# Optimization experiments

Hardware: AMD Instinct MI355X
Metric: run time of the kernel (lower is better)

The kernel has to match this reference:

```python
import jax, jax.numpy as jnp
import numpy as np

BITS = 8
GROUP_SIZE = 32


def setup_inputs() -> dict:
    key = jax.random.key(0)
    k_x, k_w, k_b = jax.random.split(key, 3)
    out_f, in_f = 4096, 4096
    num_groups = in_f // GROUP_SIZE
    x = jax.random.normal(k_x, (4, 2048, in_f), dtype=jnp.float32)
    orig_weight = jax.random.normal(k_w, (out_f, in_f), dtype=jnp.float32)
    value = jnp.zeros((out_f, in_f), dtype=jnp.float32)
    min_scale = jnp.ones((out_f, num_groups), dtype=jnp.float32)
    max_scale = jnp.ones((out_f, num_groups), dtype=jnp.float32)
    bias = jax.random.normal(k_b, (out_f,), dtype=jnp.float32)
    return {"x": x, "orig_weight": orig_weight, "value": value,
            "min_scale": min_scale, "max_scale": max_scale, "bias": bias}


def _dequant_weight(orig_weight, value, min_scale, max_scale):
    out_f, in_f = orig_weight.shape
    num_groups = in_f // GROUP_SIZE
    max_val = (1 << BITS) - 1
    wg = orig_weight.reshape(out_f, num_groups, GROUP_SIZE)
    w_min = jnp.min(wg, axis=-1, keepdims=True) * min_scale[..., None]
    w_max = jnp.max(wg, axis=-1, keepdims=True) * max_scale[..., None]
    scale = jnp.maximum((w_max - w_min) / max_val, 1e-8)
    zero_point = -w_min / scale
    ws = wg / scale + zero_point + value.reshape(out_f, num_groups, GROUP_SIZE)
    wq = jnp.clip(jnp.round(ws), 0.0, float(max_val))
    return (scale * (wq - zero_point)).reshape(out_f, in_f)


def reference(x, orig_weight, value, min_scale, max_scale, bias):
    # group-wise learnable fake-quant dequantization of the weight, then linear
    weight_dq = _dequant_weight(orig_weight, value, min_scale, max_scale)  # [out, in]
    return jnp.einsum('bsi,oi->bso', x, weight_dq) + bias
```

## Files before the change

kernel.cpp:

```cpp
#include <hip/hip_runtime.h>

#define M_DIM 8192
#define N_DIM 4096
#define K_DIM 4096
#define GROUPS_PER_ROW 128
#define NT (K_DIM / 64)

typedef short bf16x8 __attribute__((ext_vector_type(8)));
typedef float f32x4  __attribute__((ext_vector_type(4)));
typedef unsigned short u16x8 __attribute__((ext_vector_type(8)));

__device__ __forceinline__ unsigned short f2bf(float f) {
    unsigned int u = __float_as_uint(f);
    u += 0x7fffu + ((u >> 16) & 1u);
    return (unsigned short)(u >> 16);
}

typedef const __attribute__((address_space(1))) void gvoid_t;
typedef __attribute__((address_space(3))) void lvoid_t;
__device__ __forceinline__ void gload_lds16(const void* g, void* l) {
    __builtin_amdgcn_global_load_lds((gvoid_t*)g, (lvoid_t*)l, 16, 0, 0);
}

__global__ __launch_bounds__(256) void dequant_kernel(
        const float* __restrict__ w, const float* __restrict__ value,
        const float* __restrict__ mins, const float* __restrict__ maxs,
        unsigned short* __restrict__ wq) {
    int g = blockIdx.x * 256 + threadIdx.x;
    const float4* wp = reinterpret_cast<const float4*>(w + (size_t)g * 32);
    const float4* vp = reinterpret_cast<const float4*>(value + (size_t)g * 32);
    float4 wv[8], vv[8];
    #pragma unroll
    for (int j = 0; j < 8; j++) { wv[j] = wp[j]; vv[j] = vp[j]; }
    float mn = wv[0].x, mx = wv[0].x;
    #pragma unroll
    for (int j = 0; j < 8; j++) {
        mn = fminf(mn, fminf(fminf(wv[j].x, wv[j].y), fminf(wv[j].z, wv[j].w)));
        mx = fmaxf(mx, fmaxf(fmaxf(wv[j].x, wv[j].y), fmaxf(wv[j].z, wv[j].w)));
    }
    float w_min = mn * mins[g];
    float w_max = mx * maxs[g];
    float scale = fmaxf((w_max - w_min) * (1.0f / 255.0f), 1e-8f);
    float zp    = -w_min / scale;
    float rs    = 1.0f / scale;
    unsigned short ob[32];
    #pragma unroll
    for (int j = 0; j < 8; j++) {
        const float* wf = &wv[j].x;
        const float* vf = &vv[j].x;
        #pragma unroll
        for (int c = 0; c < 4; c++) {
            float ws_ = wf[c] * rs + zp + vf[c];
            float q   = fminf(fmaxf(rintf(ws_), 0.0f), 255.0f);
            ob[j * 4 + c] = f2bf(scale * (q - zp));
        }
    }
    u16x8* op = reinterpret_cast<u16x8*>(wq + (size_t)g * 32);
    #pragma unroll
    for (int j = 0; j < 4; j++) {
        u16x8 v;
        #pragma unroll
        for (int c = 0; c < 8; c++) v[c] = ob[j * 8 + c];
        op[j] = v;
    }
}

__global__ __launch_bounds__(256) void xconv_kernel(
        const float* __restrict__ x, unsigned short* __restrict__ xb) {
    int t = blockIdx.x * 256 + threadIdx.x;
    const float4* xp = reinterpret_cast<const float4*>(x) + (size_t)t * 2;
    float4 a = xp[0], b = xp[1];
    u16x8 v;
    v[0] = f2bf(a.x); v[1] = f2bf(a.y); v[2] = f2bf(a.z); v[3] = f2bf(a.w);
    v[4] = f2bf(b.x); v[5] = f2bf(b.y); v[6] = f2bf(b.z); v[7] = f2bf(b.w);
    reinterpret_cast<u16x8*>(xb)[t] = v;
}

__global__ __launch_bounds__(512, 2) void gemm_kernel(
        const unsigned short* __restrict__ A, const unsigned short* __restrict__ B,
        const float* __restrict__ bias, float* __restrict__ C) {
    __shared__ __align__(128) char lds[131072];

    const int tid  = threadIdx.x;
    const int lane = tid & 63;
    const int w    = tid >> 6;
    const int wr   = w >> 2;
    const int wc   = w & 3;
    const int l15  = lane & 15, lk = lane >> 4;

    const int bid = blockIdx.x;
    const int swz = (bid & 7) * 64 + (bid >> 3);
    const int bm  = swz >> 4;
    const int bn  = swz & 15;

    const int swb   = ((l15 >> 3) & 1) << 5;
    const int rbyte = ((l15 * 64 + lk * 16) ^ swb);
    const int abase = wr * 16384 + rbyte;
    const int bbase = 32768 + (wc >> 1) * 16384 + (wc & 1) * 4096 + rbyte;

    const int c0  = tid * 16;
    const int c1  = 8192 + tid * 16;
    const int lb0 = c0 ^ (((c0 >> 9) & 1) << 5);
    const int lb1 = c1 ^ (((c1 >> 9) & 1) << 5);
    const int so0 = ((lb0 >> 6) & 127) * (K_DIM * 2) + (lb0 >> 13) * 64 + (lb0 & 63);
    const int so1 = ((lb1 >> 6) & 127) * (K_DIM * 2) + (lb1 >> 13) * 64 + (lb1 & 63);

    const char* srcA0 = (const char*)A + (size_t)(bm * 256 +   0) * (K_DIM * 2);
    const char* srcA1 = (const char*)A + (size_t)(bm * 256 + 128) * (K_DIM * 2);
    const char* srcB0 = (const char*)B + (size_t)(bn * 256 +   0) * (K_DIM * 2);
    const char* srcB1 = (const char*)B + (size_t)(bn * 256 + 128) * (K_DIM * 2);

    char* ldsc = (char*)lds;
    auto STAGE = [&](const char* src, int tt, int regionOff) {
        gload_lds16(src + (size_t)tt * 128 + so0, ldsc + regionOff + c0);
        gload_lds16(src + (size_t)tt * 128 + so1, ldsc + regionOff + c1);
    };

    f32x4 acc[8][4] = {};
    bf16x8 af[4][2], bf_[4][2];

    STAGE(srcA0, 0, 0);
    STAGE(srcA1, 0, 16384);
    STAGE(srcB0, 0, 32768);
    STAGE(srcB1, 0, 49152);
    STAGE(srcA0, 1, 65536);
    STAGE(srcA1, 1, 65536 + 16384);
    asm volatile("s_waitcnt vmcnt(4)" ::: "memory");
    __builtin_amdgcn_s_barrier();
    __builtin_amdgcn_sched_barrier(0);

    #pragma unroll 2
    for (int t = 0; t < NT; ++t) {
        const int bo  = (t & 1) << 16;
        const int bo2 = bo ^ 65536;

        #pragma unroll
        for (int mi = 0; mi < 4; ++mi)
            #pragma unroll
            for (int kk = 0; kk < 2; ++kk)
                af[mi][kk] = *(const bf16x8*)(ldsc + bo + abase + mi * 1024 + kk * 8192);
        #pragma unroll
        for (int ni = 0; ni < 2; ++ni)
            #pragma unroll
            for (int kk = 0; kk < 2; ++kk)
                bf_[ni][kk] = *(const bf16x8*)(ldsc + bo + bbase + ni * 1024 + kk * 8192);
        if (t + 1 < NT) STAGE(srcB0, t + 1, bo2 + 32768);
        __builtin_amdgcn_s_barrier();
        __builtin_amdgcn_sched_barrier(0);
        __builtin_amdgcn_s_setprio(1);
        #pragma unroll
        for (int mi = 0; mi < 4; ++mi)
            #pragma unroll
            for (int ni = 0; ni < 2; ++ni)
                #pragma unroll
                for (int kk = 0; kk < 2; ++kk)
                    acc[mi][ni] = __builtin_amdgcn_mfma_f32_16x16x32_bf16(
                        af[mi][kk], bf_[ni][kk], acc[mi][ni], 0, 0, 0);
        __builtin_amdgcn_s_setprio(0);

        #pragma unroll
        for (int ni = 2; ni < 4; ++ni)
            #pragma unroll
            for (int kk = 0; kk < 2; ++kk)
                bf_[ni][kk] = *(const bf16x8*)(ldsc + bo + bbase + ni * 1024 + kk * 8192);
        if (t + 1 < NT) STAGE(srcB1, t + 1, bo2 + 49152);
        __builtin_amdgcn_s_barrier();
        __builtin_amdgcn_sched_barrier(0);
        __builtin_amdgcn_s_setprio(1);
        #pragma unroll
        for (int mi = 0; mi < 4; ++mi)
            #pragma unroll
            for (int ni = 2; ni < 4; ++ni)
                #pragma unroll
                for (int kk = 0; kk < 2; ++kk)
                    acc[mi][ni] = __builtin_amdgcn_mfma_f32_16x16x32_bf16(
                        af[mi][kk], bf_[ni][kk], acc[mi][ni], 0, 0, 0);
        __builtin_amdgcn_s_setprio(0);

        #pragma unroll
        for (int mi = 0; mi < 4; ++mi)
            #pragma unroll
            for (int kk = 0; kk < 2; ++kk)
                af[mi][kk] = *(const bf16x8*)(ldsc + bo + abase + 4096 + mi * 1024 + kk * 8192);
        if (t + 2 < NT) {
            STAGE(srcA0, t + 2, bo + 0);
            STAGE(srcA1, t + 2, bo + 16384);
        }
        __builtin_amdgcn_s_barrier();
        __builtin_amdgcn_sched_barrier(0);
        __builtin_amdgcn_s_setprio(1);
        #pragma unroll
        for (int mi = 0; mi < 4; ++mi)
            #pragma unroll
            for (int ni = 2; ni < 4; ++ni)
                #pragma unroll
                for (int kk = 0; kk < 2; ++kk)
                    acc[mi + 4][ni] = __builtin_amdgcn_mfma_f32_16x16x32_bf16(
                        af[mi][kk], bf_[ni][kk], acc[mi + 4][ni], 0, 0, 0);
        #pragma unroll
        for (int mi = 0; mi < 4; ++mi)
            #pragma unroll
            for (int ni = 0; ni < 2; ++ni)
                #pragma unroll
                for (int kk = 0; kk < 2; ++kk)
                    acc[mi + 4][ni] = __builtin_amdgcn_mfma_f32_16x16x32_bf16(
                        af[mi][kk], bf_[ni][kk], acc[mi + 4][ni], 0, 0, 0);
        __builtin_amdgcn_s_setprio(0);
        if (t + 2 < NT)      { asm volatile("s_waitcnt vmcnt(4)" ::: "memory"); }
        else if (t + 1 < NT) { asm volatile("s_waitcnt vmcnt(0)" ::: "memory"); }
        __builtin_amdgcn_s_barrier();
        __builtin_amdgcn_sched_barrier(0);
    }

    float bv[4];
    #pragma unroll
    for (int ni = 0; ni < 4; ++ni)
        bv[ni] = bias[bn * 256 + wc * 64 + ni * 16 + l15];
    #pragma unroll
    for (int mi = 0; mi < 8; ++mi) {
        const int m0 = bm * 256 + wr * 128 + mi * 16 + lk * 4;
        #pragma unroll
        for (int ni = 0; ni < 4; ++ni) {
            const int n = bn * 256 + wc * 64 + ni * 16 + l15;
            #pragma unroll
            for (int r = 0; r < 4; ++r)
                C[(size_t)(m0 + r) * N_DIM + n] = acc[mi][ni][r] + bv[ni];
        }
    }
}

__global__ __launch_bounds__(256) void fallback_gemm(
        const float* __restrict__ x, const float* __restrict__ w,
        const float* __restrict__ value, const float* __restrict__ mins,
        const float* __restrict__ maxs, const float* __restrict__ bias,
        float* __restrict__ out) {
    const int n = blockIdx.x;
    __shared__ float wrow[K_DIM];
    const int tid = threadIdx.x;
    if (tid < GROUPS_PER_ROW) {
        const int g = tid;
        const float* wp = w + (size_t)n * K_DIM + g * 32;
        const float* vp = value + (size_t)n * K_DIM + g * 32;
        float tw[32];
        float mn = 1e30f, mx = -1e30f;
        #pragma unroll
        for (int j = 0; j < 32; j++) {
            tw[j] = wp[j]; mn = fminf(mn, tw[j]); mx = fmaxf(mx, tw[j]);
        }
        float wmin = mn * mins[n * GROUPS_PER_ROW + g];
        float wmax = mx * maxs[n * GROUPS_PER_ROW + g];
        float scale = fmaxf((wmax - wmin) * (1.0f / 255.0f), 1e-8f);
        float zp = -wmin / scale;
        #pragma unroll
        for (int j = 0; j < 32; j++) {
            float ws_ = tw[j] / scale + zp + vp[j];
            float q = fminf(fmaxf(rintf(ws_), 0.0f), 255.0f);
            wrow[g * 32 + j] = scale * (q - zp);
        }
    }
    __syncthreads();
    const float bv = bias[n];
    for (int m = tid; m < M_DIM; m += 256) {
        const float4* xr = reinterpret_cast<const float4*>(x + (size_t)m * K_DIM);
        const float4* wr4 = reinterpret_cast<const float4*>(wrow);
        float s = 0.f;
        for (int k = 0; k < K_DIM / 4; k++) {
            float4 a = xr[k], b = wr4[k];
            s += a.x * b.x + a.y * b.y + a.z * b.z + a.w * b.w;
        }
        out[(size_t)m * N_DIM + n] = s + bv;
    }
}

extern "C" void kernel_launch(void* const* d_in, const int* in_sizes, int n_in,
                              void* d_out, int out_size, void* d_ws, size_t ws_size,
                              hipStream_t stream) {
    const float* x     = (const float*)d_in[0];
    const float* ow    = (const float*)d_in[1];
    const float* value = (const float*)d_in[2];
    const float* mins  = (const float*)d_in[3];
    const float* maxs  = (const float*)d_in[4];
    const float* bias  = (const float*)d_in[5];
    float* out = (float*)d_out;

    const size_t xb_bytes = (size_t)M_DIM * K_DIM * 2;
    const size_t wb_bytes = (size_t)N_DIM * K_DIM * 2;

    if (ws_size >= xb_bytes + wb_bytes) {
        unsigned short* xb = (unsigned short*)d_ws;
        unsigned short* wb = (unsigned short*)((char*)d_ws + xb_bytes);

        dequant_kernel<<<(N_DIM * GROUPS_PER_ROW) / 256, 256, 0, stream>>>(
            ow, value, mins, maxs, wb);
        xconv_kernel<<<(M_DIM * K_DIM / 8) / 256, 256, 0, stream>>>(x, xb);
        gemm_kernel<<<(M_DIM / 256) * (N_DIM / 256), 512, 0, stream>>>(
            xb, wb, bias, out);
    } else {
        fallback_gemm<<<N_DIM, 256, 0, stream>>>(x, ow, value, mins, maxs, bias, out);
    }
}
```

Baseline: 288.5 us.

## Switch GEMM inner tiles from 16x16x32 to 32x32x16 bf16 MFMA

Replaces the 16x16x32 MFMA micro-tiles with 32x32x16 MFMA instructions, reorganizing per-wave accumulators into 4x2 blocks of 16-float vectors and rewriting the LDS fragment addressing and swizzle for the new operand layout. The larger MFMA shape needs fewer LDS fragment reads per FLOP and fewer instructions, aiming to reduce LDS bandwidth pressure and issue overhead. The epilogue store mapping is updated to the 32x32 output layout. It risks LDS bank conflicts under the new access pattern and different register pressure.

```diff
diff --git a/kernel.cpp b/kernel.cpp
--- a/kernel.cpp
+++ b/kernel.cpp
@@ -7,7 +7,7 @@
 #define NT (K_DIM / 64)
 
 typedef short bf16x8 __attribute__((ext_vector_type(8)));
-typedef float f32x4  __attribute__((ext_vector_type(4)));
+typedef float f32x16 __attribute__((ext_vector_type(16)));
 typedef unsigned short u16x8 __attribute__((ext_vector_type(8)));
 
 __device__ __forceinline__ unsigned short f2bf(float f) {
@@ -86,17 +86,18 @@
     const int w    = tid >> 6;
     const int wr   = w >> 2;
     const int wc   = w & 3;
-    const int l15  = lane & 15, lk = lane >> 4;
+    const int l31  = lane & 31, l5 = lane >> 5;
 
     const int bid = blockIdx.x;
     const int swz = (bid & 7) * 64 + (bid >> 3);
     const int bm  = swz >> 4;
     const int bn  = swz & 15;
 
-    const int swb   = ((l15 >> 3) & 1) << 5;
-    const int rbyte = ((l15 * 64 + lk * 16) ^ swb);
-    const int abase = wr * 16384 + rbyte;
-    const int bbase = 32768 + (wc >> 1) * 16384 + (wc & 1) * 4096 + rbyte;
+    const int amask = (l31 & 8) << 2;
+    const int ib    = l5 * 16;
+
+    const int aoff = wr * 16384 + l31 * 64;
+    const int boff = 32768 + (wc >> 1) * 16384 + (wc & 1) * 4096 + l31 * 64;
 
     const int c0  = tid * 16;
     const int c1  = 8192 + tid * 16;
@@ -116,8 +117,9 @@
         gload_lds16(src + (size_t)tt * 128 + so1, ldsc + regionOff + c1);
     };
 
-    f32x4 acc[8][4] = {};
-    bf16x8 af[4][2], bf_[4][2];
+    f32x16 acc[4][2] = {};
+    bf16x8 af[2][4], bfA[4], bfB[4];
+
 
     STAGE(srcA0, 0, 0);
     STAGE(srcA1, 0, 16384);
@@ -135,53 +137,49 @@
         const int bo2 = bo ^ 65536;
 
         #pragma unroll
-        for (int mi = 0; mi < 4; ++mi)
-            #pragma unroll
-            for (int kk = 0; kk < 2; ++kk)
-                af[mi][kk] = *(const bf16x8*)(ldsc + bo + abase + mi * 1024 + kk * 8192);
-        #pragma unroll
-        for (int ni = 0; ni < 2; ++ni)
-            #pragma unroll
-            for (int kk = 0; kk < 2; ++kk)
-                bf_[ni][kk] = *(const bf16x8*)(ldsc + bo + bbase + ni * 1024 + kk * 8192);
+        for (int mb = 0; mb < 2; ++mb)
+            #pragma unroll
+            for (int kb = 0; kb < 4; ++kb)
+                af[mb][kb] = *(const bf16x8*)(ldsc + bo + aoff + mb * 2048
+                                + (kb >> 1) * 8192 + (((kb & 1) * 32) ^ amask) + ib);
+        #pragma unroll
+        for (int kb = 0; kb < 4; ++kb)
+            bfA[kb] = *(const bf16x8*)(ldsc + bo + boff
+                                + (kb >> 1) * 8192 + (((kb & 1) * 32) ^ amask) + ib);
         if (t + 1 < NT) STAGE(srcB0, t + 1, bo2 + 32768);
         __builtin_amdgcn_s_barrier();
         __builtin_amdgcn_sched_barrier(0);
         __builtin_amdgcn_s_setprio(1);
         #pragma unroll
-        for (int mi = 0; mi < 4; ++mi)
-            #pragma unroll
-            for (int ni = 0; ni < 2; ++ni)
-                #pragma unroll
-                for (int kk = 0; kk < 2; ++kk)
-                    acc[mi][ni] = __builtin_amdgcn_mfma_f32_16x16x32_bf16(
-                        af[mi][kk], bf_[ni][kk], acc[mi][ni], 0, 0, 0);
+        for (int mb = 0; mb < 2; ++mb)
+            #pragma unroll
+            for (int kb = 0; kb < 4; ++kb)
+                acc[mb][0] = __builtin_amdgcn_mfma_f32_32x32x16_bf16(
+                    af[mb][kb], bfA[kb], acc[mb][0], 0, 0, 0);
         __builtin_amdgcn_s_setprio(0);
 
         #pragma unroll
-        for (int ni = 2; ni < 4; ++ni)
-            #pragma unroll
-            for (int kk = 0; kk < 2; ++kk)
-                bf_[ni][kk] = *(const bf16x8*)(ldsc + bo + bbase + ni * 1024 + kk * 8192);
+        for (int kb = 0; kb < 4; ++kb)
+            bfB[kb] = *(const bf16x8*)(ldsc + bo + boff + 2048
+                                + (kb >> 1) * 8192 + (((kb & 1) * 32) ^ amask) + ib);
         if (t + 1 < NT) STAGE(srcB1, t + 1, bo2 + 49152);
         __builtin_amdgcn_s_barrier();
         __builtin_amdgcn_sched_barrier(0);
         __builtin_amdgcn_s_setprio(1);
         #pragma unroll
-        for (int mi = 0; mi < 4; ++mi)
-            #pragma unroll
-            for (int ni = 2; ni < 4; ++ni)
-                #pragma unroll
-                for (int kk = 0; kk < 2; ++kk)
-                    acc[mi][ni] = __builtin_amdgcn_mfma_f32_16x16x32_bf16(
-                        af[mi][kk], bf_[ni][kk], acc[mi][ni], 0, 0, 0);
+        for (int mb = 0; mb < 2; ++mb)
+            #pragma unroll
+            for (int kb = 0; kb < 4; ++kb)
+                acc[mb][1] = __builtin_amdgcn_mfma_f32_32x32x16_bf16(
+                    af[mb][kb], bfB[kb], acc[mb][1], 0, 0, 0);
         __builtin_amdgcn_s_setprio(0);
 
         #pragma unroll
-        for (int mi = 0; mi < 4; ++mi)
-            #pragma unroll
-            for (int kk = 0; kk < 2; ++kk)
-                af[mi][kk] = *(const bf16x8*)(ldsc + bo + abase + 4096 + mi * 1024 + kk * 8192);
+        for (int mb = 0; mb < 2; ++mb)
+            #pragma unroll
+            for (int kb = 0; kb < 4; ++kb)
+                af[mb][kb] = *(const bf16x8*)(ldsc + bo + aoff + (mb + 2) * 2048
+                                + (kb >> 1) * 8192 + (((kb & 1) * 32) ^ amask) + ib);
         if (t + 2 < NT) {
             STAGE(srcA0, t + 2, bo + 0);
             STAGE(srcA1, t + 2, bo + 16384);
@@ -190,21 +188,17 @@
         __builtin_amdgcn_sched_barrier(0);
         __builtin_amdgcn_s_setprio(1);
         #pragma unroll
-        for (int mi = 0; mi < 4; ++mi)
-            #pragma unroll
-            for (int ni = 2; ni < 4; ++ni)
-                #pragma unroll
-                for (int kk = 0; kk < 2; ++kk)
-                    acc[mi + 4][ni] = __builtin_amdgcn_mfma_f32_16x16x32_bf16(
-                        af[mi][kk], bf_[ni][kk], acc[mi + 4][ni], 0, 0, 0);
-        #pragma unroll
-        for (int mi = 0; mi < 4; ++mi)
-            #pragma unroll
-            for (int ni = 0; ni < 2; ++ni)
-                #pragma unroll
-                for (int kk = 0; kk < 2; ++kk)
-                    acc[mi + 4][ni] = __builtin_amdgcn_mfma_f32_16x16x32_bf16(
-                        af[mi][kk], bf_[ni][kk], acc[mi + 4][ni], 0, 0, 0);
+        for (int mb = 0; mb < 2; ++mb)
+            #pragma unroll
+            for (int kb = 0; kb < 4; ++kb)
+                acc[mb + 2][1] = __builtin_amdgcn_mfma_f32_32x32x16_bf16(
+                    af[mb][kb], bfB[kb], acc[mb + 2][1], 0, 0, 0);
+        #pragma unroll
+        for (int mb = 0; mb < 2; ++mb)
+            #pragma unroll
+            for (int kb = 0; kb < 4; ++kb)
+                acc[mb + 2][0] = __builtin_amdgcn_mfma_f32_32x32x16_bf16(
+                    af[mb][kb], bfA[kb], acc[mb + 2][0], 0, 0, 0);
         __builtin_amdgcn_s_setprio(0);
         if (t + 2 < NT)      { asm volatile("s_waitcnt vmcnt(4)" ::: "memory"); }
         else if (t + 1 < NT) { asm volatile("s_waitcnt vmcnt(0)" ::: "memory"); }
@@ -212,19 +206,21 @@
         __builtin_amdgcn_sched_barrier(0);
     }
 
-    float bv[4];
-    #pragma unroll
-    for (int ni = 0; ni < 4; ++ni)
-        bv[ni] = bias[bn * 256 + wc * 64 + ni * 16 + l15];
-    #pragma unroll
-    for (int mi = 0; mi < 8; ++mi) {
-        const int m0 = bm * 256 + wr * 128 + mi * 16 + lk * 4;
-        #pragma unroll
-        for (int ni = 0; ni < 4; ++ni) {
-            const int n = bn * 256 + wc * 64 + ni * 16 + l15;
-            #pragma unroll
-            for (int r = 0; r < 4; ++r)
-                C[(size_t)(m0 + r) * N_DIM + n] = acc[mi][ni][r] + bv[ni];
+    float bv[2];
+    #pragma unroll
+    for (int nb = 0; nb < 2; ++nb)
+        bv[nb] = bias[bn * 256 + wc * 64 + nb * 32 + l31];
+    #pragma unroll
+    for (int mb = 0; mb < 4; ++mb) {
+        const int rbase = bm * 256 + wr * 128 + mb * 32 + 4 * l5;
+        #pragma unroll
+        for (int nb = 0; nb < 2; ++nb) {
+            const int col = bn * 256 + wc * 64 + nb * 32 + l31;
+            #pragma unroll
+            for (int r = 0; r < 16; ++r) {
+                const int row = rbase + (r & 3) + 8 * (r >> 2);
+                C[(size_t)row * N_DIM + col] = acc[mb][nb][r] + bv[nb];
+            }
         }
     }
 }
```

After: 321.6 us. +11.5%, slower.

## Load GEMM B operand directly from global into registers, staging only A in LDS

Applied to the files above, without the earlier changes.

The B (weight) tile no longer goes through LDS. Each wave now reads its B fragments straight from global memory into registers every k-step, while only A is staged in LDS. This halves the shared-memory footprint and drops the B staging and barrier phases. The block-to-tile mapping is also changed to a simpler interleave. In exchange, waves that share B columns issue duplicate global loads, and a full vmcnt(0) wait each iteration exposes global latency, since A is now only single-step prefetched.

```diff
diff --git a/kernel.cpp b/kernel.cpp
--- a/kernel.cpp
+++ b/kernel.cpp
@@ -79,7 +79,7 @@
 __global__ __launch_bounds__(512, 2) void gemm_kernel(
         const unsigned short* __restrict__ A, const unsigned short* __restrict__ B,
         const float* __restrict__ bias, float* __restrict__ C) {
-    __shared__ __align__(128) char lds[131072];
+    __shared__ __align__(128) char lds[65536];
 
     const int tid  = threadIdx.x;
     const int lane = tid & 63;
@@ -89,14 +89,12 @@
     const int l15  = lane & 15, lk = lane >> 4;
 
     const int bid = blockIdx.x;
-    const int swz = (bid & 7) * 64 + (bid >> 3);
-    const int bm  = swz >> 4;
-    const int bn  = swz & 15;
+    const int bn  = (bid & 7) * 2 + ((bid >> 3) & 1);
+    const int bm  = bid >> 4;
 
     const int swb   = ((l15 >> 3) & 1) << 5;
     const int rbyte = ((l15 * 64 + lk * 16) ^ swb);
     const int abase = wr * 16384 + rbyte;
-    const int bbase = 32768 + (wc >> 1) * 16384 + (wc & 1) * 4096 + rbyte;
 
     const int c0  = tid * 16;
     const int c1  = 8192 + tid * 16;
@@ -107,8 +105,6 @@
 
     const char* srcA0 = (const char*)A + (size_t)(bm * 256 +   0) * (K_DIM * 2);
     const char* srcA1 = (const char*)A + (size_t)(bm * 256 + 128) * (K_DIM * 2);
-    const char* srcB0 = (const char*)B + (size_t)(bn * 256 +   0) * (K_DIM * 2);
-    const char* srcB1 = (const char*)B + (size_t)(bn * 256 + 128) * (K_DIM * 2);
 
     char* ldsc = (char*)lds;
     auto STAGE = [&](const char* src, int tt, int regionOff) {
@@ -116,98 +112,77 @@
         gload_lds16(src + (size_t)tt * 128 + so1, ldsc + regionOff + c1);
     };
 
+    const unsigned short* bG = B + (size_t)(bn * 256 + wc * 64 + l15) * K_DIM + lk * 8;
+
     f32x4 acc[8][4] = {};
-    bf16x8 af[4][2], bf_[4][2];
+    bf16x8 bf_[4][2];
 
     STAGE(srcA0, 0, 0);
     STAGE(srcA1, 0, 16384);
-    STAGE(srcB0, 0, 32768);
-    STAGE(srcB1, 0, 49152);
-    STAGE(srcA0, 1, 65536);
-    STAGE(srcA1, 1, 65536 + 16384);
-    asm volatile("s_waitcnt vmcnt(4)" ::: "memory");
+    asm volatile("s_waitcnt vmcnt(0)" ::: "memory");
     __builtin_amdgcn_s_barrier();
     __builtin_amdgcn_sched_barrier(0);
 
     #pragma unroll 2
     for (int t = 0; t < NT; ++t) {
-        const int bo  = (t & 1) << 16;
-        const int bo2 = bo ^ 65536;
-
-        #pragma unroll
-        for (int mi = 0; mi < 4; ++mi)
+        const int bo  = (t & 1) << 15;
+        const int bo2 = bo ^ 32768;
+
+        #pragma unroll
+        for (int ni = 0; ni < 4; ++ni)
             #pragma unroll
             for (int kk = 0; kk < 2; ++kk)
-                af[mi][kk] = *(const bf16x8*)(ldsc + bo + abase + mi * 1024 + kk * 8192);
-        #pragma unroll
-        for (int ni = 0; ni < 2; ++ni)
-            #pragma unroll
-            for (int kk = 0; kk < 2; ++kk)
-                bf_[ni][kk] = *(const bf16x8*)(ldsc + bo + bbase + ni * 1024 + kk * 8192);
-        if (t + 1 < NT) STAGE(srcB0, t + 1, bo2 + 32768);
+                bf_[ni][kk] = *(const bf16x8*)(bG + (size_t)ni * 16 * K_DIM
+                                               + t * 64 + kk * 32);
+        if (t + 1 < NT) STAGE(srcA0, t + 1, bo2);
+
+        #pragma unroll
+        for (int p = 0; p < 2; ++p) {
+            bf16x8 af[2][2];
+            #pragma unroll
+            for (int i = 0; i < 2; ++i)
+                #pragma unroll
+                for (int kk = 0; kk < 2; ++kk)
+                    af[i][kk] = *(const bf16x8*)(ldsc + bo + abase
+                                    + (p * 2 + i) * 1024 + kk * 8192);
+            __builtin_amdgcn_s_setprio(1);
+            #pragma unroll
+            for (int i = 0; i < 2; ++i)
+                #pragma unroll
+                for (int ni = 0; ni < 4; ++ni)
+                    #pragma unroll
+                    for (int kk = 0; kk < 2; ++kk)
+                        acc[p * 2 + i][ni] = __builtin_amdgcn_mfma_f32_16x16x32_bf16(
+                            af[i][kk], bf_[ni][kk], acc[p * 2 + i][ni], 0, 0, 0);
+            __builtin_amdgcn_s_setprio(0);
+        }
+
+        if (t + 1 < NT) STAGE(srcA1, t + 1, bo2 + 16384);
         __builtin_amdgcn_s_barrier();
         __builtin_amdgcn_sched_barrier(0);
-        __builtin_amdgcn_s_setprio(1);
-        #pragma unroll
-        for (int mi = 0; mi < 4; ++mi)
-            #pragma unroll
-            for (int ni = 0; ni < 2; ++ni)
+
+        #pragma unroll
+        for (int p = 2; p < 4; ++p) {
+            bf16x8 af[2][2];
+            #pragma unroll
+            for (int i = 0; i < 2; ++i)
                 #pragma unroll
                 for (int kk = 0; kk < 2; ++kk)
-                    acc[mi][ni] = __builtin_amdgcn_mfma_f32_16x16x32_bf16(
-                        af[mi][kk], bf_[ni][kk], acc[mi][ni], 0, 0, 0);
-        __builtin_amdgcn_s_setprio(0);
-
-        #pragma unroll
-        for (int ni = 2; ni < 4; ++ni)
-            #pragma unroll
-            for (int kk = 0; kk < 2; ++kk)
-                bf_[ni][kk] = *(const bf16x8*)(ldsc + bo + bbase + ni * 1024 + kk * 8192);
-        if (t + 1 < NT) STAGE(srcB1, t + 1, bo2 + 49152);
-        __builtin_amdgcn_s_barrier();
-        __builtin_amdgcn_sched_barrier(0);
-        __builtin_amdgcn_s_setprio(1);
-        #pragma unroll
-        for (int mi = 0; mi < 4; ++mi)
-            #pragma unroll
-            for (int ni = 2; ni < 4; ++ni)
-                #pragma unroll
-                for (int kk = 0; kk < 2; ++kk)
-                    acc[mi][ni] = __builtin_amdgcn_mfma_f32_16x16x32_bf16(
-                        af[mi][kk], bf_[ni][kk], acc[mi][ni], 0, 0, 0);
-        __builtin_amdgcn_s_setprio(0);
-
-        #pragma unroll
-        for (int mi = 0; mi < 4; ++mi)
-            #pragma unroll
-            for (int kk = 0; kk < 2; ++kk)
-                af[mi][kk] = *(const bf16x8*)(ldsc + bo + abase + 4096 + mi * 1024 + kk * 8192);
-        if (t + 2 < NT) {
-            STAGE(srcA0, t + 2, bo + 0);
-            STAGE(srcA1, t + 2, bo + 16384);
-        }
-        __builtin_amdgcn_s_barrier();
-        __builtin_amdgcn_sched_barrier(0);
-        __builtin_amdgcn_s_setprio(1);
-        #pragma unroll
-        for (int mi = 0; mi < 4; ++mi)
-            #pragma unroll
-            for (int ni = 2; ni < 4; ++ni)
-                #pragma unroll
-                for (int kk = 0; kk < 2; ++kk)
-                    acc[mi + 4][ni] = __builtin_amdgcn_mfma_f32_16x16x32_bf16(
-                        af[mi][kk], bf_[ni][kk], acc[mi + 4][ni], 0, 0, 0);
-        #pragma unroll
-        for (int mi = 0; mi < 4; ++mi)
-            #pragma unroll
-            for (int ni = 0; ni < 2; ++ni)
-                #pragma unroll
-                for (int kk = 0; kk < 2; ++kk)
-                    acc[mi + 4][ni] = __builtin_amdgcn_mfma_f32_16x16x32_bf16(
-                        af[mi][kk], bf_[ni][kk], acc[mi + 4][ni], 0, 0, 0);
-        __builtin_amdgcn_s_setprio(0);
-        if (t + 2 < NT)      { asm volatile("s_waitcnt vmcnt(4)" ::: "memory"); }
-        else if (t + 1 < NT) { asm volatile("s_waitcnt vmcnt(0)" ::: "memory"); }
+                    af[i][kk] = *(const bf16x8*)(ldsc + bo + abase
+                                    + (p * 2 + i) * 1024 + kk * 8192);
+            __builtin_amdgcn_s_setprio(1);
+            #pragma unroll
+            for (int i = 0; i < 2; ++i)
+                #pragma unroll
+                for (int ni = 0; ni < 4; ++ni)
+                    #pragma unroll
+                    for (int kk = 0; kk < 2; ++kk)
+                        acc[p * 2 + i][ni] = __builtin_amdgcn_mfma_f32_16x16x32_bf16(
+                            af[i][kk], bf_[ni][kk], acc[p * 2 + i][ni], 0, 0, 0);
+            __builtin_amdgcn_s_setprio(0);
+        }
+
+        asm volatile("s_waitcnt vmcnt(0)" ::: "memory");
         __builtin_amdgcn_s_barrier();
         __builtin_amdgcn_sched_barrier(0);
     }
```

After: 487.3 us. +68.9%, slower.
